# Optimization experiments

Measured on AMD Instinct MI355X. Metric: run time of the kernel, lower is better.

## Reference

```python
import jax, jax.numpy as jnp
import numpy as np

NV = 8192   # vertices_number
NF = 16384  # number of faces (~2*nv for a closed mesh)
BATCH = 32


def build_laplacian(faces, nv):
    """Faithful jax translation of the torch constructor's dense Laplacian."""
    f0, f1, f2 = faces[:, 0], faces[:, 1], faces[:, 2]
    rows = jnp.concatenate([f0, f1, f1, f2, f2, f0])
    cols = jnp.concatenate([f1, f0, f2, f1, f0, f2])
    L = jnp.zeros((nv, nv), jnp.float32)
    # torch uses assignment (=-1), duplicates overwrite -> .set, not .add
    L = L.at[rows, cols].set(-1.0)
    diag = -L.sum(axis=1)  # degree on the diagonal
    idx = jnp.arange(nv)
    L = L.at[idx, idx].set(diag)
    # row-normalize rows whose diagonal is nonzero
    safe = jnp.where(diag != 0, diag, 1.0)[:, None]
    L = jnp.where((diag != 0)[:, None], L / safe, L)
    return L


def setup_inputs() -> dict:
    key = jax.random.key(0)
    k1, k2 = jax.random.split(key)
    x = jax.random.normal(k1, (BATCH, NV, 3), dtype=jnp.float32)
    faces = jax.random.randint(k2, (NF, 3), 0, NV)
    return {"x": x, "faces": faces}


def reference(x, faces):
    nv = x.shape[1]
    L = build_laplacian(faces, nv)          # [nv, nv]
    y = jnp.einsum('vw,bwd->bvd', L, x)     # dense matmul, as the torch module does
    # pow(2).sum over all non-batch dims, divided by nv; average=False -> per-batch
    return jnp.sum(y * y, axis=(1, 2)) / nv
```

## Files before the change

kernel.cpp:

```cpp
#include <hip/hip_runtime.h>

#define NV 8192
#define NF 16384
#define BATCH 32
#define VPB 32
#define WORDS 256
#define MAXD 64

typedef unsigned short ushort_t;

__global__ __launch_bounds__(1024)
void build_kernel(const int* __restrict__ faces,
                  unsigned* __restrict__ info,
                  ushort_t* __restrict__ nbr,
                  int* __restrict__ counter) {
    __shared__ unsigned bits[VPB][WORDS];

    const int t    = threadIdx.x;
    const int base = blockIdx.x * VPB;

    uint4* bz = reinterpret_cast<uint4*>(&bits[0][0]);
    bz[t]        = make_uint4(0, 0, 0, 0);
    bz[t + 1024] = make_uint4(0, 0, 0, 0);
    if (blockIdx.x == 0 && t == 0) *counter = 0;
    __syncthreads();

    const uint4* f4 = reinterpret_cast<const uint4*>(faces);
    #define SETB(vi, w) atomicOr(&bits[vi][(int)(w) >> 5], 1u << ((w) & 31))
    #define PROC(a, b, c) { \
        const unsigned ra = (unsigned)((int)(a) - base); \
        const unsigned rb = (unsigned)((int)(b) - base); \
        const unsigned rc = (unsigned)((int)(c) - base); \
        if (ra < VPB) { SETB(ra, (b)); SETB(ra, (c)); } \
        if (rb < VPB) { SETB(rb, (a)); SETB(rb, (c)); } \
        if (rc < VPB) { SETB(rc, (b)); SETB(rc, (a)); } }
    #pragma unroll
    for (int i = 0; i < NF / 4096; ++i) {
        const int j = (i * 1024 + t) * 3;
        const uint4 p = f4[j], q = f4[j + 1], r = f4[j + 2];
        PROC(p.x, p.y, p.z);
        PROC(p.w, q.x, q.y);
        PROC(q.z, q.w, r.x);
        PROC(r.y, r.z, r.w);
    }
    #undef PROC
    #undef SETB
    __syncthreads();

    const int lane = t & 63;
    const int wid  = t >> 6;
    #pragma unroll
    for (int s = 0; s < 2; ++s) {
        const int vi = wid * 2 + s;
        const int v  = base + vi;

        const uint4 wq = reinterpret_cast<const uint4*>(&bits[vi][0])[lane];
        unsigned wm[4] = {wq.x, wq.y, wq.z, wq.w};

        int pc = __popc(wm[0]) + __popc(wm[1]) + __popc(wm[2]) + __popc(wm[3]);

        const int selfword = v >> 5;
        const int wbase0   = lane * 4;
        int c = pc;
        if (selfword >= wbase0 && selfword < wbase0 + 4) {
            const unsigned m = 1u << (v & 31);
            if (wm[selfword - wbase0] & m) { wm[selfword - wbase0] &= ~m; c -= 1; }
        }

        int incl = c;
        #pragma unroll
        for (int off = 1; off < 64; off <<= 1) {
            int o = __shfl_up(incl, off);
            if (lane >= off) incl += o;
        }
        const int ofs     = incl - c;
        const int total_c = __shfl(incl, 63);

        int pct = pc;
        #pragma unroll
        for (int off = 1; off < 64; off <<= 1) pct += __shfl_xor(pct, off);

        int idx = ofs;
        #pragma unroll
        for (int jw = 0; jw < 4; ++jw) {
            unsigned bb = wm[jw];
            const int wb = (wbase0 + jw) << 5;
            while (bb) {
                const int bpos = __ffs(bb) - 1;
                bb &= bb - 1;
                if (idx < MAXD) nbr[(size_t)v * MAXD + idx] = (ushort_t)(wb + bpos);
                ++idx;
            }
        }
        if (lane == 0)
            info[v] = (unsigned)pct |
                      ((unsigned)(total_c < MAXD ? total_c : MAXD) << 16);
    }
}

__global__ __launch_bounds__(1024)
void gather_kernel(const float* __restrict__ x,
                   const unsigned* __restrict__ info,
                   const ushort_t* __restrict__ nbr,
                   float* __restrict__ partials,
                   int* __restrict__ counter,
                   float* __restrict__ out) {
    __shared__ float lx[NV * 3];
    __shared__ float red[16];
    __shared__ int isLast;

    const int t = threadIdx.x;
    const int b = blockIdx.x >> 3;
    const int g = blockIdx.x & 7;

    const float4* xs = reinterpret_cast<const float4*>(x + (size_t)b * NV * 3);
    float4* ls = reinterpret_cast<float4*>(lx);
    #pragma unroll
    for (int i = 0; i < 6; ++i) ls[t + i * 1024] = xs[t + i * 1024];

    const int v = g * 1024 + t;
    const unsigned iv = info[v];
    const int dv = (int)(iv & 0xFFFFu);
    const int cv = (int)(iv >> 16);

    const uint4* np = reinterpret_cast<const uint4*>(nbr + (size_t)v * MAXD);
    const uint4 n0 = np[0], n1 = np[1], n2 = np[2], n3 = np[3];
    const unsigned nd[16] = {n0.x, n0.y, n0.z, n0.w,
                             n1.x, n1.y, n1.z, n1.w,
                             n2.x, n2.y, n2.z, n2.w,
                             n3.x, n3.y, n3.z, n3.w};

    int kmax = cv;
    #pragma unroll
    for (int off = 1; off < 64; off <<= 1) {
        int o = __shfl_xor(kmax, off);
        kmax = kmax > o ? kmax : o;
    }

    __syncthreads();

    float s0 = 0.f, s1 = 0.f, s2 = 0.f;
    #pragma unroll
    for (int k = 0; k < 32; ++k) {
        if (k >= kmax) break;
        if (k < cv) {
            const int w = (int)((nd[k >> 1] >> ((k & 1) * 16)) & 0xFFFFu) * 3;
            s0 += lx[w];
            s1 += lx[w + 1];
            s2 += lx[w + 2];
        }
    }
    if (kmax > 32) {
        for (int k = 32; k < cv; ++k) {
            const int w = (int)nbr[(size_t)v * MAXD + k] * 3;
            s0 += lx[w];
            s1 += lx[w + 1];
            s2 += lx[w + 2];
        }
    }

    float r = 0.f;
    if (dv > 0) {
        const float inv = 1.0f / (float)dv;
        const float y0 = lx[v * 3]     - s0 * inv;
        const float y1 = lx[v * 3 + 1] - s1 * inv;
        const float y2 = lx[v * 3 + 2] - s2 * inv;
        r = y0 * y0 + y1 * y1 + y2 * y2;
    }

    #pragma unroll
    for (int off = 32; off > 0; off >>= 1) r += __shfl_down(r, off);
    if ((t & 63) == 0) red[t >> 6] = r;
    __syncthreads();

    if (t == 0) {
        float s = 0.f;
        #pragma unroll
        for (int i = 0; i < 16; ++i) s += red[i];
        __hip_atomic_store(&partials[blockIdx.x], s,
                           __ATOMIC_RELAXED, __HIP_MEMORY_SCOPE_AGENT);
        int old = __hip_atomic_fetch_add(counter, 1,
                                         __ATOMIC_ACQ_REL, __HIP_MEMORY_SCOPE_AGENT);
        isLast = (old == (int)gridDim.x - 1);
    }
    __syncthreads();

    if (isLast && t < BATCH) {
        float s = 0.f;
        #pragma unroll
        for (int gg = 0; gg < 8; ++gg)
            s += __hip_atomic_load(&partials[t * 8 + gg],
                                   __ATOMIC_RELAXED, __HIP_MEMORY_SCOPE_AGENT);
        out[t] = s / (float)NV;
    }
}

extern "C" void kernel_launch(void* const* d_in, const int* in_sizes, int n_in,
                              void* d_out, int out_size, void* d_ws, size_t ws_size,
                              hipStream_t stream) {
    const float* x   = (const float*)d_in[0];
    const int* faces = (const int*)d_in[1];
    float* out       = (float*)d_out;

    char* ws = (char*)d_ws;
    ushort_t* nbr     = (ushort_t*)ws;
    unsigned* info    = (unsigned*)(ws + (size_t)MAXD * NV * 2);
    int*      counter = (int*)(info + NV);
    float*    partials= (float*)(counter + 64);

    build_kernel <<<NV / VPB, 1024, 0, stream>>>(faces, info, nbr, counter);
    gather_kernel<<<BATCH * 8, 1024, 0, stream>>>(x, info, nbr, partials, counter, out);
}
```

Measured before the change: 24.51 us.

## Repack x to float4 in build kernel and use float4 LDS gathers

The build kernel now also converts x from packed xyz triples into a padded float4 array in workspace, and the gather kernel loads that into shared memory as float4 and reads each neighbour with a single 16-byte LDS load instead of three scalar loads. VPB is doubled to 64, which halves the build grid to 128 blocks so each block covers exactly the 262144 x elements. The cost is an extra global write and read of a 4 MB padded copy of x, plus more shared-memory bit arrays per build block.

After: 33.60 us. +37.1%, slower.

```diff
diff --git a/kernel.cpp b/kernel.cpp
--- a/kernel.cpp
+++ b/kernel.cpp
@@ -3,7 +3,7 @@
 #define NV 8192
 #define NF 16384
 #define BATCH 32
-#define VPB 32
+#define VPB 64
 #define WORDS 256
 #define MAXD 64
 
@@ -11,6 +11,8 @@
 
 __global__ __launch_bounds__(1024)
 void build_kernel(const int* __restrict__ faces,
+                  const float* __restrict__ x,
+                  float4* __restrict__ x4,
                   unsigned* __restrict__ info,
                   ushort_t* __restrict__ nbr,
                   int* __restrict__ counter) {
@@ -18,10 +20,18 @@
 
     const int t    = threadIdx.x;
     const int base = blockIdx.x * VPB;
+    const int gid  = blockIdx.x * 1024 + t;
+
+    #pragma unroll
+    for (int s = 0; s < 2; ++s) {
+        const int slot = gid + s * 131072;
+        const float* src = x + (size_t)slot * 3;
+        x4[slot] = make_float4(src[0], src[1], src[2], 0.f);
+    }
 
     uint4* bz = reinterpret_cast<uint4*>(&bits[0][0]);
-    bz[t]        = make_uint4(0, 0, 0, 0);
-    bz[t + 1024] = make_uint4(0, 0, 0, 0);
+    #pragma unroll
+    for (int k = 0; k < 4; ++k) bz[t + k * 1024] = make_uint4(0, 0, 0, 0);
     if (blockIdx.x == 0 && t == 0) *counter = 0;
     __syncthreads();
 
@@ -50,8 +60,8 @@
     const int lane = t & 63;
     const int wid  = t >> 6;
     #pragma unroll
-    for (int s = 0; s < 2; ++s) {
-        const int vi = wid * 2 + s;
+    for (int s = 0; s < 4; ++s) {
+        const int vi = wid * 4 + s;
         const int v  = base + vi;
 
         const uint4 wq = reinterpret_cast<const uint4*>(&bits[vi][0])[lane];
@@ -99,13 +109,13 @@
 }
 
 __global__ __launch_bounds__(1024)
-void gather_kernel(const float* __restrict__ x,
+void gather_kernel(const float4* __restrict__ x4,
                    const unsigned* __restrict__ info,
                    const ushort_t* __restrict__ nbr,
                    float* __restrict__ partials,
                    int* __restrict__ counter,
                    float* __restrict__ out) {
-    __shared__ float lx[NV * 3];
+    __shared__ float4 lx4[NV];
     __shared__ float red[16];
     __shared__ int isLast;
 
@@ -113,10 +123,9 @@
     const int b = blockIdx.x >> 3;
     const int g = blockIdx.x & 7;
 
-    const float4* xs = reinterpret_cast<const float4*>(x + (size_t)b * NV * 3);
-    float4* ls = reinterpret_cast<float4*>(lx);
-    #pragma unroll
-    for (int i = 0; i < 6; ++i) ls[t + i * 1024] = xs[t + i * 1024];
+    const float4* xs = x4 + (size_t)b * NV;
+    #pragma unroll
+    for (int i = 0; i < 8; ++i) lx4[t + i * 1024] = xs[t + i * 1024];
 
     const int v = g * 1024 + t;
     const unsigned iv = info[v];
@@ -144,27 +153,25 @@
     for (int k = 0; k < 32; ++k) {
         if (k >= kmax) break;
         if (k < cv) {
-            const int w = (int)((nd[k >> 1] >> ((k & 1) * 16)) & 0xFFFFu) * 3;
-            s0 += lx[w];
-            s1 += lx[w + 1];
-            s2 += lx[w + 2];
+            const int w = (int)((nd[k >> 1] >> ((k & 1) * 16)) & 0xFFFFu);
+            const float4 q = lx4[w];
+            s0 += q.x; s1 += q.y; s2 += q.z;
         }
     }
     if (kmax > 32) {
         for (int k = 32; k < cv; ++k) {
-            const int w = (int)nbr[(size_t)v * MAXD + k] * 3;
-            s0 += lx[w];
-            s1 += lx[w + 1];
-            s2 += lx[w + 2];
+            const float4 q = lx4[(int)nbr[(size_t)v * MAXD + k]];
+            s0 += q.x; s1 += q.y; s2 += q.z;
         }
     }
 
     float r = 0.f;
     if (dv > 0) {
         const float inv = 1.0f / (float)dv;
-        const float y0 = lx[v * 3]     - s0 * inv;
-        const float y1 = lx[v * 3 + 1] - s1 * inv;
-        const float y2 = lx[v * 3 + 2] - s2 * inv;
+        const float4 sv = lx4[v];
+        const float y0 = sv.x - s0 * inv;
+        const float y1 = sv.y - s1 * inv;
+        const float y2 = sv.z - s2 * inv;
         r = y0 * y0 + y1 * y1 + y2 * y2;
     }
 
@@ -203,11 +210,12 @@
     float* out       = (float*)d_out;
 
     char* ws = (char*)d_ws;
-    ushort_t* nbr     = (ushort_t*)ws;
-    unsigned* info    = (unsigned*)(ws + (size_t)MAXD * NV * 2);
+    float4*   x4      = (float4*)ws;
+    ushort_t* nbr     = (ushort_t*)(ws + (size_t)BATCH * NV * 16);
+    unsigned* info    = (unsigned*)((char*)nbr + (size_t)MAXD * NV * 2);
     int*      counter = (int*)(info + NV);
     float*    partials= (float*)(counter + 64);
 
-    build_kernel <<<NV / VPB, 1024, 0, stream>>>(faces, info, nbr, counter);
-    gather_kernel<<<BATCH * 8, 1024, 0, stream>>>(x, info, nbr, partials, counter, out);
+    build_kernel <<<NV / VPB, 1024, 0, stream>>>(faces, x, x4, info, nbr, counter);
+    gather_kernel<<<BATCH * 8, 1024, 0, stream>>>(x4, info, nbr, partials, counter, out);
 }
```
